# Kernel optimization log

Measured on AMD Instinct MI355X. Metric: run time of the kernel, lower is better.

Reference implementation:

```python
import jax, jax.numpy as jnp
import numpy as np

HID = 4096; H = 32; KVH = 8; D = 128
B = 4; Q = 256; KV = 2048; HIST = KV - Q
BS = 64; NB = KV // BS; NBLOCKS = 160
WINDOW = 1024; THETA = 10000.0


def _rope(x, pos):
    # x: [T, heads, D], pos: [T] absolute positions
    half = D // 2
    inv = 1.0 / (THETA ** (jnp.arange(half, dtype=jnp.float32) / half))
    f = pos.astype(jnp.float32)[:, None] * inv[None, :]          # [T, D/2]
    cos = jnp.concatenate([jnp.cos(f), jnp.cos(f)], -1)[:, None, :]
    sin = jnp.concatenate([jnp.sin(f), jnp.sin(f)], -1)[:, None, :]
    x1, x2 = jnp.split(x, 2, axis=-1)
    return x * cos + jnp.concatenate([-x2, x1], -1) * sin


def setup_inputs() -> dict:
    key = jax.random.key(0)
    ks = jax.random.split(key, 7)
    T = B * Q
    return dict(
        hidden_states=jax.random.normal(ks[0], (T, HID), jnp.float32),
        wq=jax.random.normal(ks[1], (HID, H * D), jnp.float32) * 0.02,
        wk=jax.random.normal(ks[2], (HID, KVH * D), jnp.float32) * 0.02,
        wv=jax.random.normal(ks[3], (HID, KVH * D), jnp.float32) * 0.02,
        wo=jax.random.normal(ks[4], (H * D, HID), jnp.float32) * 0.02,
        k_cache=jax.random.normal(ks[5], (NBLOCKS, BS, KVH, D), jnp.float32),
        v_cache=jax.random.normal(ks[6], (NBLOCKS, BS, KVH, D), jnp.float32),
        # each sequence appends Q new tokens at positions [HIST, KV)
        position_ids=jnp.tile(HIST + jnp.arange(Q, dtype=jnp.int32), B),
        q_start_loc=jnp.arange(B, dtype=jnp.int32) * Q,
        q_seq_length=jnp.full((B,), Q, jnp.int32),
        kv_seq_length=jnp.full((B,), KV, jnp.int32),
        block_offsets=jnp.arange(B * NB, dtype=jnp.int32).reshape(B, NB),
    )


def reference(hidden_states, wq, wk, wv, wo, k_cache, v_cache,
              position_ids, q_start_loc, q_seq_length, kv_seq_length,
              block_offsets):
    # qkv proj (no bias, Mistral)
    q = (hidden_states @ wq).reshape(-1, H, D)    # [T, H, D]
    k = (hidden_states @ wk).reshape(-1, KVH, D)  # [T, KVH, D]
    v = (hidden_states @ wv).reshape(-1, KVH, D)
    # rotary embedding on q, k with per-token absolute positions
    q = _rope(q, position_ids)
    k = _rope(k, position_ids)
    # fill paged KV cache: token with in-sequence slot s of sequence b goes to
    # block block_offsets[b, s // BS], offset s % BS
    b_idx = jnp.repeat(jnp.arange(B), Q)
    blk = block_offsets[b_idx, position_ids // BS]
    off = position_ids % BS
    k_cache = k_cache.at[blk, off].set(k)
    v_cache = v_cache.at[blk, off].set(v)
    # paged attention: gather each sequence's blocks from the cache
    k_all = k_cache[block_offsets].reshape(B, KV, KVH, D)
    v_all = v_cache[block_offsets].reshape(B, KV, KVH, D)
    G = H // KVH  # GQA group size
    qb = q.reshape(B, Q, KVH, G, D)
    scores = jnp.einsum('bqhgd,bkhd->bhgqk', qb, k_all) / jnp.sqrt(jnp.float32(D))
    # causal + sliding-window mask on absolute positions
    qpos = HIST + jnp.arange(Q)
    kpos = jnp.arange(KV)
    valid = (kpos[None, :] <= qpos[:, None]) & (kpos[None, :] > qpos[:, None] - WINDOW)
    scores = jnp.where(valid[None, None, None], scores, -jnp.inf)
    p = jax.nn.softmax(scores, axis=-1)
    o = jnp.einsum('bhgqk,bkhd->bqhgd', p, v_all).reshape(B * Q, H * D)
    return o @ wo
```

## Files before the change

### kernel.cpp

```cpp
#include <hip/hip_runtime.h>

#define BSZ  4
#define QL   256
#define KVL  2048
#define HIST 1792
#define WIN  1024
#define NH   32
#define NKVH 8
#define DH   128
#define HID  4096
#define SCALE 0.088388347648318447f
#define MFIX  8.0f

typedef __bf16 bf16x8 __attribute__((ext_vector_type(8)));
typedef float  fx4    __attribute__((ext_vector_type(4)));
typedef unsigned short us4 __attribute__((ext_vector_type(4)));
typedef unsigned short us8 __attribute__((ext_vector_type(8)));

__device__ __forceinline__ unsigned short f2bf(float x) {
    unsigned u = __float_as_uint(x);
    u += 0x7FFFu + ((u >> 16) & 1u);
    return (unsigned short)(u >> 16);
}
__device__ __forceinline__ float bf2f(unsigned short h) {
    return __uint_as_float(((unsigned)h) << 16);
}
__device__ __forceinline__ fx4 mfma16(bf16x8 a, bf16x8 b, fx4 c) {
    return __builtin_amdgcn_mfma_f32_16x16x32_bf16(a, b, c, 0, 0, 0);
}
__device__ __forceinline__ bf16x8 ldb16(const unsigned short* p) {
    return *reinterpret_cast<const bf16x8*>(p);
}

typedef __attribute__((address_space(1))) const void gv_t;
typedef __attribute__((address_space(3))) void lv_t;
__device__ __forceinline__ void gl16(const void* g, void* l) {
    __builtin_amdgcn_global_load_lds((gv_t*)g, (lv_t*)l, 16, 0, 0);
}

template<int TAG>
__global__ __launch_bounds__(256) void gemm_bf16_kernel(
    const unsigned short* __restrict__ A, const unsigned short* __restrict__ B,
    float* __restrict__ C0, float* __restrict__ Cz, size_t czstride,
    int lda, int ldb, int ldc, int ksteps, int klast, int nx, int ny, int nz)
{
    constexpr int TILE = 128 * 32;
    __shared__ __align__(16) unsigned short lds[3 * 2 * TILE];

    const int per = gridDim.x >> 3;
    const int t = (blockIdx.x & 7) * per + (blockIdx.x >> 3);
    const int bx = t % nx;
    const int by = (t / nx) % ny;
    const int bz = t / (nx * ny);

    const int row0 = bx * 128;
    const int col0 = by * 128;
    const int kbase = bz * ksteps * 32;
    const int nks = (bz == nz - 1) ? klast : ksteps;
    float* Cm = (bz == 0) ? C0 : (Cz + (size_t)(bz - 1) * czstride);

    const int tid  = threadIdx.x;
    const int lane = tid & 63;
    const int w    = tid >> 6;
    const int wr   = w >> 1, wc = w & 1;
    const int l16  = lane & 15;
    const int lg   = lane >> 4;
    const int r_in = lane >> 2;
    const int c8   = (lane & 3) * 8;

    fx4 acc[4][4] = {};

    auto STAGE = [&](int bufi, int kp) {
        unsigned short* Lb = lds + bufi * (2 * TILE);
#pragma unroll
        for (int i = 0; i < 2; ++i) {
            const int r = w * 32 + i * 16 + r_in;
            const int ldsb = (w * 2 + i) * 512;
            gl16(A + (size_t)(row0 + r) * lda + kp + c8, Lb + ldsb);
            gl16(B + (size_t)(col0 + r) * ldb + kp + c8, Lb + TILE + ldsb);
        }
    };

    STAGE(0, kbase);
    STAGE(1, kbase + 32);
    for (int ks = 0; ks < nks; ++ks) {
        if (ks + 2 < nks) {
            STAGE((ks + 2) % 3, kbase + (ks + 2) * 32);
            asm volatile("s_waitcnt vmcnt(8)" ::: "memory");
        } else if (ks + 1 < nks) {
            asm volatile("s_waitcnt vmcnt(4)" ::: "memory");
        } else {
            asm volatile("s_waitcnt vmcnt(0)" ::: "memory");
        }
        __builtin_amdgcn_s_barrier();
        __builtin_amdgcn_sched_barrier(0);

        const unsigned short* Lb = lds + (ks % 3) * (2 * TILE);
        const unsigned short* AhT = Lb;
        const unsigned short* BhT = Lb + TILE;

        bf16x8 af[4], bfv[4];
#pragma unroll
        for (int f = 0; f < 4; ++f) {
            af[f]  = ldb16(AhT + (wr * 64 + f * 16 + l16) * 32 + lg * 8);
            bfv[f] = ldb16(BhT + (wc * 64 + f * 16 + l16) * 32 + lg * 8);
        }
        __builtin_amdgcn_s_setprio(1);
#pragma unroll
        for (int fr = 0; fr < 4; ++fr)
#pragma unroll
            for (int fc = 0; fc < 4; ++fc)
                acc[fr][fc] = mfma16(af[fr], bfv[fc], acc[fr][fc]);
        __builtin_amdgcn_s_setprio(0);
        __builtin_amdgcn_sched_barrier(0);
        __builtin_amdgcn_s_barrier();
    }
#pragma unroll
    for (int fr = 0; fr < 4; ++fr)
#pragma unroll
        for (int fc = 0; fc < 4; ++fc) {
            const size_t rbase = (size_t)(row0 + wr * 64 + fr * 16 + lg * 4);
            const int col = col0 + wc * 64 + fc * 16 + l16;
#pragma unroll
            for (int r = 0; r < 4; ++r)
                Cm[(rbase + r) * ldc + col] = acc[fr][fc][r];
        }
}

__global__ __launch_bounds__(256) void transpose_w_kernel(
    const float* __restrict__ w, unsigned short* __restrict__ hi, int N)
{
    __shared__ unsigned short sh[64][72];
    const int n0 = blockIdx.x * 64;
    const int k0 = blockIdx.y * 64;
    const int tid = threadIdx.x;
    const int rr = tid >> 4;
    const int cc = (tid & 15) * 4;
#pragma unroll
    for (int p = 0; p < 4; ++p) {
        const int kl = p * 16 + rr;
        fx4 v = *reinterpret_cast<const fx4*>(w + (size_t)(k0 + kl) * N + n0 + cc);
#pragma unroll
        for (int j = 0; j < 4; ++j)
            sh[cc + j][kl] = f2bf(v[j]);
    }
    __syncthreads();
    const int nl = tid >> 2;
    const int kc = (tid & 3) * 16;
    unsigned short* oh = hi + (size_t)(n0 + nl) * 4096 + k0 + kc;
    *reinterpret_cast<us8*>(oh)     = *reinterpret_cast<const us8*>(&sh[nl][kc]);
    *reinterpret_cast<us8*>(oh + 8) = *reinterpret_cast<const us8*>(&sh[nl][kc + 8]);
}

__global__ __launch_bounds__(256) void convert_bf16_kernel(
    const float* __restrict__ in, unsigned short* __restrict__ out, int n4)
{
    int i = blockIdx.x * blockDim.x + threadIdx.x;
    for (; i < n4; i += gridDim.x * blockDim.x) {
        fx4 v = reinterpret_cast<const fx4*>(in)[i];
        us4 o;
#pragma unroll
        for (int j = 0; j < 4; ++j) o[j] = f2bf(v[j]);
        reinterpret_cast<us4*>(out)[i] = o;
    }
}

__global__ void sincos_table_kernel(float* __restrict__ tab)
{
    const int qi = blockIdx.x;
    const int jr = threadIdx.x;
    const float inv = powf(10000.f, -(float)jr * (1.f / 64.f));
    const float f = (float)(HIST + qi) * inv;
    float s, c;
    sincosf(f, &s, &c);
    tab[(qi * 64 + jr) * 2]     = c;
    tab[(qi * 64 + jr) * 2 + 1] = s;
}

__global__ __launch_bounds__(256) void rope_q_kernel(
    const float* __restrict__ qkv0, const float* __restrict__ qkv1,
    const int* __restrict__ pos_ids, const float* __restrict__ tab,
    unsigned short* __restrict__ qb)
{
    const int t = blockIdx.x;
    const int b = t >> 8;
    const int qi = t & 255;
    const int pi = pos_ids[t] - HIST;
    const int tid = threadIdx.x;
    const int h = tid >> 3;
    const int d0 = (tid & 7) * 8;
    const float* q0 = qkv0 + (size_t)t * 6144 + h * DH;
    const float* q1 = qkv1 + (size_t)t * 6144 + h * DH;
    float xl[8], xh[8];
    *reinterpret_cast<fx4*>(&xl[0]) = *reinterpret_cast<const fx4*>(q0 + d0)
                                    + *reinterpret_cast<const fx4*>(q1 + d0);
    *reinterpret_cast<fx4*>(&xl[4]) = *reinterpret_cast<const fx4*>(q0 + d0 + 4)
                                    + *reinterpret_cast<const fx4*>(q1 + d0 + 4);
    *reinterpret_cast<fx4*>(&xh[0]) = *reinterpret_cast<const fx4*>(q0 + d0 + 64)
                                    + *reinterpret_cast<const fx4*>(q1 + d0 + 64);
    *reinterpret_cast<fx4*>(&xh[4]) = *reinterpret_cast<const fx4*>(q0 + d0 + 68)
                                    + *reinterpret_cast<const fx4*>(q1 + d0 + 68);
    us8 outl, outh;
#pragma unroll
    for (int i = 0; i < 8; ++i) {
        const int jr = d0 + i;
        const float c = tab[(pi * 64 + jr) * 2];
        const float s = tab[(pi * 64 + jr) * 2 + 1];
        outl[i] = f2bf(xl[i] * c - xh[i] * s);
        outh[i] = f2bf(xh[i] * c + xl[i] * s);
    }
    unsigned short* dst = qb + (((size_t)b * NH + h) * QL + qi) * DH;
    *reinterpret_cast<us8*>(dst + d0)      = outl;
    *reinterpret_cast<us8*>(dst + d0 + 64) = outh;
}

__global__ __launch_bounds__(256) void gather_kv_kernel(
    const float* __restrict__ qkv0, const float* __restrict__ qkv1,
    const float* __restrict__ k_cache, const float* __restrict__ v_cache,
    const int* __restrict__ block_offsets, const float* __restrict__ tab,
    unsigned short* __restrict__ k_all, unsigned short* __restrict__ vT)
{
    __shared__ unsigned short vls[32][136];
    const int bid = blockIdx.x;
    const int xcd = bid & 7;
    const int i = bid >> 3;
    const int g = ((i & 31) << 3) | xcd;
    const int kh = i >> 5;
    const int b  = g >> 6;
    const int ck = g & 63;
    const int kv0 = ck * 32;
    const int tid = threadIdx.x;
    const int tok = tid >> 3;
    const int sl  = tid & 7;
    const int kvpos = kv0 + tok;
    const bool is_old = (kvpos < HIST);

    float x[16];
    float v[16];
    if (is_old) {
        const int blk = block_offsets[b * 32 + (kvpos >> 6)];
        const size_t base = (((size_t)blk * 64 + (kvpos & 63)) * NKVH + kh) * DH + sl * 4;
        const float* sk = k_cache + base;
        const float* sv = v_cache + base;
#pragma unroll
        for (int j = 0; j < 4; ++j) {
            *reinterpret_cast<fx4*>(&x[j * 4]) = *reinterpret_cast<const fx4*>(sk + j * 32);
            *reinterpret_cast<fx4*>(&v[j * 4]) = *reinterpret_cast<const fx4*>(sv + j * 32);
        }
    } else {
        const int t = b * QL + (kvpos - HIST);
        const int pi = kvpos - HIST;
        const size_t tb = (size_t)t * 6144 + kh * DH + sl * 4;
        const float* k0p = qkv0 + tb + 4096;
        const float* k1p = qkv1 + tb + 4096;
        const float* v0p = qkv0 + tb + 5120;
        const float* v1p = qkv1 + tb + 5120;
#pragma unroll
        for (int j = 0; j < 4; ++j) {
            *reinterpret_cast<fx4*>(&x[j * 4]) =
                *reinterpret_cast<const fx4*>(k0p + j * 32) +
                *reinterpret_cast<const fx4*>(k1p + j * 32);
            *reinterpret_cast<fx4*>(&v[j * 4]) =
                *reinterpret_cast<const fx4*>(v0p + j * 32) +
                *reinterpret_cast<const fx4*>(v1p + j * 32);
        }
#pragma unroll
        for (int j = 0; j < 2; ++j) {
            const int jr0 = sl * 4 + j * 32;
            fx4 cs0 = *reinterpret_cast<const fx4*>(tab + ((size_t)pi * 64 + jr0) * 2);
            fx4 cs1 = *reinterpret_cast<const fx4*>(tab + ((size_t)pi * 64 + jr0) * 2 + 4);
            const float c[4] = {cs0[0], cs0[2], cs1[0], cs1[2]};
            const float s[4] = {cs0[1], cs0[3], cs1[1], cs1[3]};
#pragma unroll
            for (int e = 0; e < 4; ++e) {
                const float lo = x[j * 4 + e], hi = x[(j + 2) * 4 + e];
                x[j * 4 + e]       = lo * c[e] - hi * s[e];
                x[(j + 2) * 4 + e] = hi * c[e] + lo * s[e];
            }
        }
    }
    {
        const size_t tbase = (((size_t)b * NKVH + kh) * KVL + kv0) * DH;
#pragma unroll
        for (int j = 0; j < 4; ++j) {
            const int d = sl * 4 + j * 32;
            const int dc = d >> 3;
            us4 pk;
#pragma unroll
            for (int e = 0; e < 4; ++e) pk[e] = f2bf(x[j * 4 + e]);
            *reinterpret_cast<us4*>(k_all + tbase + ((dc * 32 + tok) << 3) + (d & 7)) = pk;
        }
    }
#pragma unroll
    for (int j = 0; j < 4; ++j) {
        us4 pv;
#pragma unroll
        for (int e = 0; e < 4; ++e) pv[e] = f2bf(v[j * 4 + e]);
        *reinterpret_cast<us4*>(&vls[tok][sl * 4 + j * 32]) = pv;
    }
    __syncthreads();
    const int dr = tid >> 1;
    const int half = tid & 1;
    unsigned short* vtile = vT + (((size_t)b * NKVH + kh) * 64 + ck) * 4096;
#pragma unroll
    for (int i2 = 0; i2 < 16; i2 += 8) {
        const int kvc = half * 2 + (i2 >> 3);
        us8 pk;
#pragma unroll
        for (int j = 0; j < 8; ++j) pk[j] = vls[half * 16 + i2 + j][dr];
        *reinterpret_cast<us8*>(vtile + kvc * 1024 + dr * 8) = pk;
    }
}

__global__ __launch_bounds__(512) void attn_kernel(
    const unsigned short* __restrict__ qb,
    const unsigned short* __restrict__ kall,
    const unsigned short* __restrict__ vT,
    unsigned short* __restrict__ ohi)
{
    __shared__ __align__(16) unsigned short ldskv[3 * 8192];
    __shared__ __align__(16) unsigned short plds[8][16][40];

    const int bid = blockIdx.x;
    const int xcd = bid & 7, slot = bid >> 3;
    const int pair = xcd * 4 + (slot >> 3);
    const int within = slot & 7;
    const int kh = pair >> 2, b = pair & 3;
    const int qt = within & 3, p = within >> 2;

    const int tid = threadIdx.x;
    const int lane = tid & 63;
    const int w = tid >> 6;
    const int h = kh * 4 + p * 2 + (w >> 2);
    const int ww = w & 3;
    const int l16 = lane & 15;
    const int lg = lane >> 4;
    const int qrow0 = qt * 64 + ww * 16;
    const int qabs0 = HIST + qrow0;

    const unsigned short* qptr =
        qb + (((size_t)b * NH + h) * QL + qrow0 + l16) * DH + lg * 8;
    bf16x8 qf[4];
#pragma unroll
    for (int ds = 0; ds < 4; ++ds) qf[ds] = ldb16(qptr + ds * 32);

    fx4 oacc[8];
#pragma unroll
    for (int f = 0; f < 8; ++f) oacc[f] = (fx4){0.f, 0.f, 0.f, 0.f};
    float lsum[4] = {0.f, 0.f, 0.f, 0.f};

    const unsigned short* kbase = kall + ((size_t)b * NKVH + kh) * (KVL * DH);
    const unsigned short* vbase = vT + ((size_t)b * NKVH + kh) * (KVL * DH);

    const int kv_lo = ((HIST + qt * 64) - (WIN - 1)) & ~31;

    auto STAGE = [&](int bufi, int kv0) {
        unsigned short* kl = ldskv + bufi * 8192;
        const unsigned short* kg = kbase + (size_t)kv0 * DH;
        const unsigned short* vg = vbase + (size_t)(kv0 >> 5) * 4096;
        const int ci = w * 64 + lane;
        gl16(kg + ci * 8, kl + ci * 8);
        gl16(vg + ci * 8, kl + 4096 + ci * 8);
    };

    STAGE(0, kv_lo);
    STAGE(1, kv_lo + 32);

    for (int t = 0; t < 34; ++t) {
        if (t + 2 < 34) {
            STAGE((t + 2) % 3, kv_lo + (t + 2) * 32);
            asm volatile("s_waitcnt vmcnt(4)" ::: "memory");
        } else if (t + 1 < 34) {
            asm volatile("s_waitcnt vmcnt(2)" ::: "memory");
        } else {
            asm volatile("s_waitcnt vmcnt(0)" ::: "memory");
        }
        __builtin_amdgcn_s_barrier();
        __builtin_amdgcn_sched_barrier(0);

        const unsigned short* kl = ldskv + (t % 3) * 8192;
        const unsigned short* vl = kl + 4096;
        const int kv0 = kv_lo + t * 32;

        fx4 s0 = (fx4){0.f, 0.f, 0.f, 0.f};
        fx4 s1 = (fx4){0.f, 0.f, 0.f, 0.f};
        __builtin_amdgcn_s_setprio(1);
#pragma unroll
        for (int ds = 0; ds < 4; ++ds) {
            bf16x8 kf0 = ldb16(kl + ((ds * 4 + lg) * 32 + l16) * 8);
            bf16x8 kf1 = ldb16(kl + ((ds * 4 + lg) * 32 + 16 + l16) * 8);
            s0 = mfma16(qf[ds], kf0, s0);
            s1 = mfma16(qf[ds], kf1, s1);
        }
        __builtin_amdgcn_s_setprio(0);
        float p0v[4], p1v[4];
        const bool interior = (kv0 >= qabs0 + 16 - WIN) && (kv0 + 31 <= qabs0);
        if (interior) {
#pragma unroll
            for (int r = 0; r < 4; ++r) {
                p0v[r] = __expf(fmaf(s0[r], SCALE, -MFIX));
                p1v[r] = __expf(fmaf(s1[r], SCALE, -MFIX));
            }
        } else {
            const int kvp0 = kv0 + l16, kvp1 = kvp0 + 16;
#pragma unroll
            for (int r = 0; r < 4; ++r) {
                const int qpos = qabs0 + lg * 4 + r;
                const float e0 = __expf(fmaf(s0[r], SCALE, -MFIX));
                const float e1 = __expf(fmaf(s1[r], SCALE, -MFIX));
                p0v[r] = (kvp0 <= qpos && kvp0 > qpos - WIN) ? e0 : 0.f;
                p1v[r] = (kvp1 <= qpos && kvp1 > qpos - WIN) ? e1 : 0.f;
            }
        }
#pragma unroll
        for (int r = 0; r < 4; ++r) {
            lsum[r] += p0v[r] + p1v[r];
            plds[w][lg * 4 + r][l16] = f2bf(p0v[r]);
            plds[w][lg * 4 + r][16 + l16] = f2bf(p1v[r]);
        }
        asm volatile("s_waitcnt lgkmcnt(0)" ::: "memory");
        __builtin_amdgcn_sched_barrier(0);
        bf16x8 pa = ldb16(&plds[w][l16][lg * 8]);
        __builtin_amdgcn_s_setprio(1);
#pragma unroll
        for (int f = 0; f < 8; ++f) {
            bf16x8 vf = ldb16(vl + lg * 1024 + (f * 16 + l16) * 8);
            oacc[f] = mfma16(pa, vf, oacc[f]);
        }
        __builtin_amdgcn_s_setprio(0);
        __builtin_amdgcn_sched_barrier(0);
        __builtin_amdgcn_s_barrier();
    }
#pragma unroll
    for (int r = 0; r < 4; ++r) {
#pragma unroll
        for (int off = 1; off < 16; off <<= 1)
            lsum[r] += __shfl_xor(lsum[r], off);
    }
    float rl[4];
#pragma unroll
    for (int r = 0; r < 4; ++r) rl[r] = 1.f / lsum[r];
    const size_t obase = ((size_t)b * QL + qrow0 + lg * 4) * (NH * DH) + h * DH;
#pragma unroll
    for (int f = 0; f < 8; ++f)
#pragma unroll
        for (int r = 0; r < 4; ++r)
            ohi[obase + (size_t)r * (NH * DH) + f * 16 + l16] = f2bf(oacc[f][r] * rl[r]);
}

__global__ __launch_bounds__(256) void reduce_out_kernel(
    float* __restrict__ out, const float* __restrict__ parts)
{
    const int n4 = (1024 * 4096) / 4;
    int i = blockIdx.x * blockDim.x + threadIdx.x;
    for (; i < n4; i += gridDim.x * blockDim.x) {
        fx4 v = reinterpret_cast<fx4*>(out)[i] + reinterpret_cast<const fx4*>(parts)[i];
        reinterpret_cast<fx4*>(out)[i] = v;
    }
}

extern "C" void kernel_launch(void* const* d_in, const int* in_sizes, int n_in,
                              void* d_out, int out_size, void* d_ws, size_t ws_size,
                              hipStream_t stream)
{
    const float* hs = (const float*)d_in[0];
    const float* wq = (const float*)d_in[1];
    const float* wk = (const float*)d_in[2];
    const float* wv = (const float*)d_in[3];
    const float* wo = (const float*)d_in[4];
    const float* kc = (const float*)d_in[5];
    const float* vc = (const float*)d_in[6];
    const int* pos  = (const int*)d_in[7];
    const int* boff = (const int*)d_in[11];
    float* out = (float*)d_out;

    char* ws = (char*)d_ws;
    unsigned short* woTh  = (unsigned short*)(ws + 0);
    unsigned short* wqkvT = (unsigned short*)(ws + 67108864);
    unsigned short* kall  = (unsigned short*)(ws + 67108864);
    unsigned short* vTp   = (unsigned short*)(ws + 83886080);
    unsigned short* ohi   = (unsigned short*)(ws + 100663296);
    float* qkvb           = (float*)(ws + 117440512);
    float* oparts         = (float*)(ws + 117440512);
    unsigned short* hsb   = (unsigned short*)(ws + 167772160);
    unsigned short* qbb   = (unsigned short*)(ws + 167772160);
    float* tab            = (float*)(ws + 176160768);

    transpose_w_kernel<<<dim3(64, 64), 256, 0, stream>>>(wq, wqkvT, 4096);
    transpose_w_kernel<<<dim3(16, 64), 256, 0, stream>>>(wk, wqkvT + (size_t)4096 * 4096, 1024);
    transpose_w_kernel<<<dim3(16, 64), 256, 0, stream>>>(wv, wqkvT + (size_t)5120 * 4096, 1024);
    transpose_w_kernel<<<dim3(64, 64), 256, 0, stream>>>(wo, woTh, 4096);
    convert_bf16_kernel<<<2048, 256, 0, stream>>>(hs, hsb, 1048576);
    sincos_table_kernel<<<256, 64, 0, stream>>>(tab);

    gemm_bf16_kernel<0><<<768, 256, 0, stream>>>(
        hsb, wqkvT,
        qkvb, qkvb + (size_t)1024 * 6144, (size_t)1024 * 6144,
        4096, 4096, 6144, 64, 64, 8, 48, 2);

    rope_q_kernel<<<1024, 256, 0, stream>>>(qkvb, qkvb + 6291456, pos, tab, qbb);
    gather_kv_kernel<<<2048, 256, 0, stream>>>(qkvb, qkvb + 6291456, kc, vc, boff, tab, kall, vTp);
    attn_kernel<<<256, 512, 0, stream>>>(qbb, kall, vTp, ohi);

    gemm_bf16_kernel<1><<<512, 256, 0, stream>>>(
        ohi, woTh,
        out, oparts, (size_t)1024 * 4096,
        4096, 4096, 4096, 64, 64, 8, 32, 2);
    reduce_out_kernel<<<2048, 256, 0, stream>>>(out, oparts);
}
```

Measured before the change: 248.6 us.

## Merge prep kernels into one launch and process two KV tiles per attention iteration

Folds the four weight transposes, the hidden-state bf16 conversion and the sincos table build into one prep_kernel dispatched over 12352 blocks, removing five kernel launches and the gaps between them. Separately, the attention loop now stages two 32-token KV tiles per step in a 4-slot LDS ring and runs QK, softmax and PV for both tiles between barriers, halving the barrier count and raising MFMA work per synchronization. This uses more LDS per block (4 KV buffers plus a wider P buffer), which may limit occupancy. The GEMM template is also renamed into two wrapper kernels.

```diff
diff --git a/kernel.cpp b/kernel.cpp
--- a/kernel.cpp
+++ b/kernel.cpp
@@ -38,8 +38,7 @@
     __builtin_amdgcn_global_load_lds((gv_t*)g, (lv_t*)l, 16, 0, 0);
 }
 
-template<int TAG>
-__global__ __launch_bounds__(256) void gemm_bf16_kernel(
+__device__ __forceinline__ void gemm_body(
     const unsigned short* __restrict__ A, const unsigned short* __restrict__ B,
     float* __restrict__ C0, float* __restrict__ Cz, size_t czstride,
     int lda, int ldb, int ldc, int ksteps, int klast, int nx, int ny, int nz)
@@ -127,12 +126,27 @@
         }
 }
 
-__global__ __launch_bounds__(256) void transpose_w_kernel(
-    const float* __restrict__ w, unsigned short* __restrict__ hi, int N)
+__global__ __launch_bounds__(256) void qkv_gemm_kernel(
+    const unsigned short* __restrict__ A, const unsigned short* __restrict__ B,
+    float* __restrict__ C0, float* __restrict__ Cz, size_t czstride,
+    int lda, int ldb, int ldc, int ksteps, int klast, int nx, int ny, int nz)
+{
+    gemm_body(A, B, C0, Cz, czstride, lda, ldb, ldc, ksteps, klast, nx, ny, nz);
+}
+
+__global__ __launch_bounds__(256) void oproj_gemm_kernel(
+    const unsigned short* __restrict__ A, const unsigned short* __restrict__ B,
+    float* __restrict__ C0, float* __restrict__ Cz, size_t czstride,
+    int lda, int ldb, int ldc, int ksteps, int klast, int nx, int ny, int nz)
+{
+    gemm_body(A, B, C0, Cz, czstride, lda, ldb, ldc, ksteps, klast, nx, ny, nz);
+}
+
+__device__ __forceinline__ void transpose_tile(
+    const float* __restrict__ w, unsigned short* __restrict__ hi, int N,
+    int n0, int k0)
 {
     __shared__ unsigned short sh[64][72];
-    const int n0 = blockIdx.x * 64;
-    const int k0 = blockIdx.y * 64;
     const int tid = threadIdx.x;
     const int rr = tid >> 4;
     const int cc = (tid & 15) * 4;
@@ -152,29 +166,51 @@
     *reinterpret_cast<us8*>(oh + 8) = *reinterpret_cast<const us8*>(&sh[nl][kc + 8]);
 }
 
-__global__ __launch_bounds__(256) void convert_bf16_kernel(
-    const float* __restrict__ in, unsigned short* __restrict__ out, int n4)
-{
-    int i = blockIdx.x * blockDim.x + threadIdx.x;
-    for (; i < n4; i += gridDim.x * blockDim.x) {
-        fx4 v = reinterpret_cast<const fx4*>(in)[i];
-        us4 o;
-#pragma unroll
-        for (int j = 0; j < 4; ++j) o[j] = f2bf(v[j]);
-        reinterpret_cast<us4*>(out)[i] = o;
-    }
-}
-
-__global__ void sincos_table_kernel(float* __restrict__ tab)
-{
-    const int qi = blockIdx.x;
-    const int jr = threadIdx.x;
-    const float inv = powf(10000.f, -(float)jr * (1.f / 64.f));
-    const float f = (float)(HIST + qi) * inv;
-    float s, c;
-    sincosf(f, &s, &c);
-    tab[(qi * 64 + jr) * 2]     = c;
-    tab[(qi * 64 + jr) * 2 + 1] = s;
+__global__ __launch_bounds__(256) void prep_kernel(
+    const float* __restrict__ wq, const float* __restrict__ wk,
+    const float* __restrict__ wv, const float* __restrict__ wo,
+    const float* __restrict__ hs,
+    unsigned short* __restrict__ wqkvT, unsigned short* __restrict__ woTh,
+    unsigned short* __restrict__ hsb, float* __restrict__ tab)
+{
+    const int r = blockIdx.x;
+    const int tid = threadIdx.x;
+    if (r < 4096) {
+        transpose_tile(wq, wqkvT, 4096, (r & 63) * 64, (r >> 6) * 64);
+    } else if (r < 5120) {
+        const int r2 = r - 4096;
+        transpose_tile(wk, wqkvT + (size_t)4096 * 4096, 1024,
+                       (r2 & 15) * 64, (r2 >> 4) * 64);
+    } else if (r < 6144) {
+        const int r2 = r - 5120;
+        transpose_tile(wv, wqkvT + (size_t)5120 * 4096, 1024,
+                       (r2 & 15) * 64, (r2 >> 4) * 64);
+    } else if (r < 10240) {
+        const int r2 = r - 6144;
+        transpose_tile(wo, woTh, 4096, (r2 & 63) * 64, (r2 >> 6) * 64);
+    } else if (r < 12288) {
+        const int r2 = r - 10240;
+        int i = r2 * 256 + tid;
+#pragma unroll
+        for (int rep = 0; rep < 2; ++rep) {
+            fx4 v = reinterpret_cast<const fx4*>(hs)[i];
+            us4 o;
+#pragma unroll
+            for (int j = 0; j < 4; ++j) o[j] = f2bf(v[j]);
+            reinterpret_cast<us4*>(hsb)[i] = o;
+            i += 524288;
+        }
+    } else {
+        const int r2 = r - 12288;
+        const int qi = r2 * 4 + (tid >> 6);
+        const int jr = tid & 63;
+        const float inv = powf(10000.f, -(float)jr * (1.f / 64.f));
+        const float f = (float)(HIST + qi) * inv;
+        float s, c;
+        sincosf(f, &s, &c);
+        tab[(qi * 64 + jr) * 2]     = c;
+        tab[(qi * 64 + jr) * 2 + 1] = s;
+    }
 }
 
 __global__ __launch_bounds__(256) void rope_q_kernel(
@@ -318,8 +354,8 @@
     const unsigned short* __restrict__ vT,
     unsigned short* __restrict__ ohi)
 {
-    __shared__ __align__(16) unsigned short ldskv[3 * 8192];
-    __shared__ __align__(16) unsigned short plds[8][16][40];
+    __shared__ __align__(16) unsigned short ldskv[4 * 8192];
+    __shared__ __align__(16) unsigned short plds[8][16][88];
 
     const int bid = blockIdx.x;
     const int xcd = bid & 7, slot = bid >> 3;
@@ -363,28 +399,7 @@
         gl16(vg + ci * 8, kl + 4096 + ci * 8);
     };
 
-    STAGE(0, kv_lo);
-    STAGE(1, kv_lo + 32);
-
-    for (int t = 0; t < 34; ++t) {
-        if (t + 2 < 34) {
-            STAGE((t + 2) % 3, kv_lo + (t + 2) * 32);
-            asm volatile("s_waitcnt vmcnt(4)" ::: "memory");
-        } else if (t + 1 < 34) {
-            asm volatile("s_waitcnt vmcnt(2)" ::: "memory");
-        } else {
-            asm volatile("s_waitcnt vmcnt(0)" ::: "memory");
-        }
-        __builtin_amdgcn_s_barrier();
-        __builtin_amdgcn_sched_barrier(0);
-
-        const unsigned short* kl = ldskv + (t % 3) * 8192;
-        const unsigned short* vl = kl + 4096;
-        const int kv0 = kv_lo + t * 32;
-
-        fx4 s0 = (fx4){0.f, 0.f, 0.f, 0.f};
-        fx4 s1 = (fx4){0.f, 0.f, 0.f, 0.f};
-        __builtin_amdgcn_s_setprio(1);
+    auto QK = [&](const unsigned short* kl, fx4& s0, fx4& s1) {
 #pragma unroll
         for (int ds = 0; ds < 4; ++ds) {
             bf16x8 kf0 = ldb16(kl + ((ds * 4 + lg) * 32 + l16) * 8);
@@ -392,7 +407,9 @@
             s0 = mfma16(qf[ds], kf0, s0);
             s1 = mfma16(qf[ds], kf1, s1);
         }
-        __builtin_amdgcn_s_setprio(0);
+    };
+
+    auto SM = [&](int kv0, fx4& s0, fx4& s1, int pc) {
         float p0v[4], p1v[4];
         const bool interior = (kv0 >= qabs0 + 16 - WIN) && (kv0 + 31 <= qabs0);
         if (interior) {
@@ -415,18 +432,53 @@
 #pragma unroll
         for (int r = 0; r < 4; ++r) {
             lsum[r] += p0v[r] + p1v[r];
-            plds[w][lg * 4 + r][l16] = f2bf(p0v[r]);
-            plds[w][lg * 4 + r][16 + l16] = f2bf(p1v[r]);
-        }
-        asm volatile("s_waitcnt lgkmcnt(0)" ::: "memory");
-        __builtin_amdgcn_sched_barrier(0);
-        bf16x8 pa = ldb16(&plds[w][l16][lg * 8]);
-        __builtin_amdgcn_s_setprio(1);
+            plds[w][lg * 4 + r][pc + l16] = f2bf(p0v[r]);
+            plds[w][lg * 4 + r][pc + 16 + l16] = f2bf(p1v[r]);
+        }
+    };
+
+    auto PV = [&](const unsigned short* vl, bf16x8 pa) {
 #pragma unroll
         for (int f = 0; f < 8; ++f) {
             bf16x8 vf = ldb16(vl + lg * 1024 + (f * 16 + l16) * 8);
             oacc[f] = mfma16(pa, vf, oacc[f]);
         }
+    };
+
+    STAGE(0, kv_lo);
+    STAGE(1, kv_lo + 32);
+
+    for (int t = 0; t < 34; t += 2) {
+        if (t + 2 < 34) {
+            STAGE((t + 2) & 3, kv_lo + (t + 2) * 32);
+            STAGE((t + 3) & 3, kv_lo + (t + 3) * 32);
+            asm volatile("s_waitcnt vmcnt(4)" ::: "memory");
+        } else {
+            asm volatile("s_waitcnt vmcnt(0)" ::: "memory");
+        }
+        __builtin_amdgcn_s_barrier();
+        __builtin_amdgcn_sched_barrier(0);
+
+        const unsigned short* kl0 = ldskv + (t & 3) * 8192;
+        const unsigned short* kl1 = ldskv + ((t + 1) & 3) * 8192;
+
+        fx4 sA0 = (fx4){0.f, 0.f, 0.f, 0.f}, sA1 = (fx4){0.f, 0.f, 0.f, 0.f};
+        fx4 sB0 = (fx4){0.f, 0.f, 0.f, 0.f}, sB1 = (fx4){0.f, 0.f, 0.f, 0.f};
+        __builtin_amdgcn_s_setprio(1);
+        QK(kl0, sA0, sA1);
+        QK(kl1, sB0, sB1);
+        __builtin_amdgcn_s_setprio(0);
+
+        SM(kv_lo + t * 32, sA0, sA1, 0);
+        SM(kv_lo + (t + 1) * 32, sB0, sB1, 40);
+
+        asm volatile("s_waitcnt lgkmcnt(0)" ::: "memory");
+        __builtin_amdgcn_sched_barrier(0);
+        bf16x8 pa0 = ldb16(&plds[w][l16][0 + lg * 8]);
+        bf16x8 pa1 = ldb16(&plds[w][l16][40 + lg * 8]);
+        __builtin_amdgcn_s_setprio(1);
+        PV(kl0 + 4096, pa0);
+        PV(kl1 + 4096, pa1);
         __builtin_amdgcn_s_setprio(0);
         __builtin_amdgcn_sched_barrier(0);
         __builtin_amdgcn_s_barrier();
@@ -486,14 +538,9 @@
     unsigned short* qbb   = (unsigned short*)(ws + 167772160);
     float* tab            = (float*)(ws + 176160768);
 
-    transpose_w_kernel<<<dim3(64, 64), 256, 0, stream>>>(wq, wqkvT, 4096);
-    transpose_w_kernel<<<dim3(16, 64), 256, 0, stream>>>(wk, wqkvT + (size_t)4096 * 4096, 1024);
-    transpose_w_kernel<<<dim3(16, 64), 256, 0, stream>>>(wv, wqkvT + (size_t)5120 * 4096, 1024);
-    transpose_w_kernel<<<dim3(64, 64), 256, 0, stream>>>(wo, woTh, 4096);
-    convert_bf16_kernel<<<2048, 256, 0, stream>>>(hs, hsb, 1048576);
-    sincos_table_kernel<<<256, 64, 0, stream>>>(tab);
-
-    gemm_bf16_kernel<0><<<768, 256, 0, stream>>>(
+    prep_kernel<<<12352, 256, 0, stream>>>(wq, wk, wv, wo, hs, wqkvT, woTh, hsb, tab);
+
+    qkv_gemm_kernel<<<768, 256, 0, stream>>>(
         hsb, wqkvT,
         qkvb, qkvb + (size_t)1024 * 6144, (size_t)1024 * 6144,
         4096, 4096, 6144, 64, 64, 8, 48, 2);
@@ -502,7 +549,7 @@
     gather_kv_kernel<<<2048, 256, 0, stream>>>(qkvb, qkvb + 6291456, kc, vc, boff, tab, kall, vTp);
     attn_kernel<<<256, 512, 0, stream>>>(qbb, kall, vTp, ohi);
 
-    gemm_bf16_kernel<1><<<512, 256, 0, stream>>>(
+    oproj_gemm_kernel<<<512, 256, 0, stream>>>(
         ohi, woTh,
         out, oparts, (size_t)1024 * 4096,
         4096, 4096, 4096, 64, 64, 8, 32, 2);
```

Measured after the change: 231.0 us. -7.1%, faster.
